# Kernel optimization log

Hardware: AMD Instinct MI355X
Metric: run time of the kernel (lower is better)

Reference implementation:

```python
import jax, jax.numpy as jnp
import numpy as np

N_GRID = 16       # n
CELL_SIDE = 2.0
LATENT = 16       # latent_dim (pooling_dim for type_='social')
HIDDEN = 128
OUT_DIM = 128
CONSTANT = 0.0
NUM_TRACKS = 1024


def setup_inputs() -> dict:
    key = jax.random.key(0)
    ks = jax.random.split(key, 6)
    T = NUM_TRACKS
    hidden_state = jax.random.normal(ks[0], (T, HIDDEN), jnp.float32)
    # positions spread over a ~20m scene; obs2 is obs1 plus a small step (velocity)
    obs1 = jax.random.uniform(ks[1], (T, 2), jnp.float32) * 20.0
    obs2 = obs1 + jax.random.normal(ks[2], (T, 2), jnp.float32) * 0.5
    W_enc = jax.random.normal(ks[3], (HIDDEN, LATENT), jnp.float32) / np.sqrt(HIDDEN)
    b_enc = jnp.zeros((LATENT,), jnp.float32)
    in_dim = N_GRID * N_GRID * LATENT  # 4096
    W_emb = jax.random.normal(ks[4], (in_dim, OUT_DIM), jnp.float32) / np.sqrt(in_dim)
    b_emb = jnp.zeros((OUT_DIM,), jnp.float32)
    return dict(hidden_state=hidden_state, obs1=obs1, obs2=obs2,
                W_enc=W_enc, b_enc=b_enc, W_emb=W_emb, b_emb=b_emb)


def _social_grid(hidden_state, obs2, W_enc, b_enc):
    T = obs2.shape[0]
    # NaN rows -> 0 (mask = isnan(obs).any(dim=1))
    obs = jnp.where(jnp.isnan(obs2).any(axis=1, keepdims=True), 0.0, obs2)
    # static off-diagonal neighbor indices: row i lists all j != i  [T, T-1]
    cols = np.broadcast_to(np.arange(T), (T, T))
    nbr = cols[~np.eye(T, dtype=bool)].reshape(T, T - 1)
    rel = obs[nbr] - obs[:, None, :]                 # [T, T-1, 2] obs[j]-obs[i]
    vals = hidden_state[nbr] @ W_enc + b_enc         # [T, T-1, LATENT]
    # grid cell coordinates (pool_size=1, front=False)
    oij = rel / CELL_SIDE + N_GRID / 2.0             # [T, T-1, 2]
    in_range = jnp.sum((oij < 0) | (oij >= N_GRID), axis=2) == 0  # [T, T-1]
    oij_i = jnp.where(in_range[..., None], oij, 0.0).astype(jnp.int32)
    vals = jnp.where(in_range[..., None], vals, CONSTANT)
    oi = oij_i[..., 0] * N_GRID + oij_i[..., 1]      # flat cell index [T, T-1]
    occ = jnp.full((T, N_GRID * N_GRID, LATENT), CONSTANT, vals.dtype)
    occ = occ.at[jnp.arange(T)[:, None], oi].set(vals)
    # [T, LATENT, n, n]; blur_size=1 and lp_pool with kernel=pool_size=1 are identity
    return jnp.transpose(occ, (0, 2, 1)).reshape(T, LATENT, N_GRID, N_GRID)


def reference(hidden_state, obs1, obs2, W_enc, b_enc, W_emb, b_emb):
    grid = _social_grid(hidden_state, obs2, W_enc, b_enc)
    T = grid.shape[0]
    flat = grid.reshape(T, -1)                       # [T, n*n*LATENT]
    return jax.nn.relu(flat @ W_emb + b_emb)         # [T, OUT_DIM]
```

## Files before the change

### kernel.cpp

```cpp
#include <hip/hip_runtime.h>
#include <hip/hip_bf16.h>
#include <math.h>

#define T_TRACKS 1024
#define HIDDEN 128
#define LATENT 16
#define NGRID 16
#define NCELLS 256
#define KDIM 4096
#define OUTD 128

typedef unsigned short ushort_t;
typedef __attribute__((ext_vector_type(8))) short frag_ab;
typedef __attribute__((ext_vector_type(4))) float f32x4;

static __device__ inline ushort_t f2bf(float x) {
    __hip_bfloat16 h = __float2bfloat16(x);
    return *reinterpret_cast<ushort_t*>(&h);
}

#define WS_VALS 0
#define WS_OWN  32768
#define WS_WT   557056
#define WS_PART 1605632
#define WS_NEED (1605632 + 8388608)

__global__ __launch_bounds__(256) void prep_kernel(const float* __restrict__ hidden,
                                                   const float* __restrict__ obs2,
                                                   const float* __restrict__ W_enc,
                                                   const float* __restrict__ b_enc,
                                                   const float* __restrict__ W_emb,
                                                   ushort_t* __restrict__ vals_t,
                                                   ushort_t* __restrict__ owner,
                                                   ushort_t* __restrict__ W_t) {
    const int b = blockIdx.x;
    const int tid = threadIdx.x;
    if (b < 64) {
        int idx = b * 256 + tid;
        int j = idx >> 4, l = idx & 15;
        const float* h = hidden + j * HIDDEN;
        float acc = b_enc[l];
#pragma unroll 8
        for (int k = 0; k < HIDDEN; k++) acc += h[k] * W_enc[k * LATENT + l];
        vals_t[l * T_TRACKS + j] = f2bf(acc);
    } else if (b < 320) {
        int idx = (b - 64) * 256 + tid;
        int kc = idx >> 7;
        int o = idx & 127;
        ushort_t tmp[8];
#pragma unroll
        for (int u = 0; u < 8; u++) tmp[u] = f2bf(W_emb[(kc * 8 + u) * OUTD + o]);
        *reinterpret_cast<uint4*>(W_t + o * KDIM + kc * 8) = *reinterpret_cast<uint4*>(tmp);
    } else {
        __shared__ float2 sobs[T_TRACKS];
        __shared__ int own[16][NCELLS];
        const int rbase = (b - 320) * 16;
        for (int q = tid; q < T_TRACKS; q += 256) {
            float2 o = reinterpret_cast<const float2*>(obs2)[q];
            if (isnan(o.x) || isnan(o.y)) { o.x = 0.0f; o.y = 0.0f; }
            sobs[q] = o;
        }
        for (int q = tid; q < 16 * NCELLS; q += 256) (&own[0][0])[q] = -1;
        __syncthreads();
        {
            const int r = tid & 15;
            const int i = rbase + r;
            const float oix = sobs[i].x, oiy = sobs[i].y;
            for (int j = tid >> 4; j < T_TRACKS; j += 16) {
                if (j == i) continue;
                float gx = (sobs[j].x - oix) * 0.5f + 8.0f;
                float gy = (sobs[j].y - oiy) * 0.5f + 8.0f;
                bool inr = (gx >= 0.0f) && (gx < 16.0f) && (gy >= 0.0f) && (gy < 16.0f);
                int c = inr ? ((int)gx * NGRID + (int)gy) : 0;
                atomicMax(&own[r][c], j);
            }
        }
        __syncthreads();
        for (int q = tid; q < 16 * NCELLS; q += 256) {
            int rr = q >> 8, c = q & 255;
            int j = own[rr][c];
            bool valid = (j >= 0);
            if (valid && c == 0) {
                float oix = sobs[rbase + rr].x, oiy = sobs[rbase + rr].y;
                float gx = (sobs[j].x - oix) * 0.5f + 8.0f;
                float gy = (sobs[j].y - oiy) * 0.5f + 8.0f;
                valid = (gx >= 0.0f) && (gx < 16.0f) && (gy >= 0.0f) && (gy < 16.0f);
            }
            owner[(rbase + rr) * NCELLS + c] = valid ? (ushort_t)(j + 1) : (ushort_t)0;
        }
    }
}

#define BK 128
#define LDSTR 136
__global__ __launch_bounds__(256) void gemm_kernel(const ushort_t* __restrict__ owner,
                                                   const ushort_t* __restrict__ vals_t,
                                                   const ushort_t* __restrict__ W_t,
                                                   float* __restrict__ partial) {
    const int tid = threadIdx.x;
    const int kt = blockIdx.x >> 4;
    const int mt = blockIdx.x & 15;
    const int wave = tid >> 6;
    const int lane = tid & 63;
    const int lrow = lane & 15;
    const int quad = lane >> 4;

    __shared__ ushort_t As[64 * LDSTR];
    __shared__ ushort_t Bs[128 * LDSTR];

    const ushort_t* vrow = vals_t + kt * T_TRACKS;

    f32x4 acc[8];
#pragma unroll
    for (int nt = 0; nt < 8; nt++) acc[nt] = (f32x4){0.f, 0.f, 0.f, 0.f};

    for (int chunk = 0; chunk < 2; chunk++) {
        const int c0 = chunk * BK;
        for (int q = tid; q < 2048; q += 256) {
            int r = q >> 5, c4 = (q & 31) * 4;
            ushort4 o4 = *reinterpret_cast<const ushort4*>(owner + (mt * 64 + r) * NCELLS + c0 + c4);
            ushort4 v;
            v.x = o4.x ? vrow[o4.x - 1] : (ushort_t)0;
            v.y = o4.y ? vrow[o4.y - 1] : (ushort_t)0;
            v.z = o4.z ? vrow[o4.z - 1] : (ushort_t)0;
            v.w = o4.w ? vrow[o4.w - 1] : (ushort_t)0;
            *reinterpret_cast<ushort4*>(As + r * LDSTR + c4) = v;
        }
        for (int g = tid; g < 2048; g += 256) {
            int n = g >> 4, cs = g & 15;
            uint4 v = *reinterpret_cast<const uint4*>(W_t + n * KDIM + kt * 256 + c0 + cs * 8);
            *reinterpret_cast<uint4*>(Bs + n * LDSTR + cs * 8) = v;
        }
        __syncthreads();
#pragma unroll
        for (int ks = 0; ks < 4; ks++) {
            const int koff = ks * 32 + quad * 8;
            frag_ab a = *reinterpret_cast<const frag_ab*>(&As[(wave * 16 + lrow) * LDSTR + koff]);
#pragma unroll
            for (int nt = 0; nt < 8; nt++) {
                frag_ab bfr = *reinterpret_cast<const frag_ab*>(&Bs[(nt * 16 + lrow) * LDSTR + koff]);
                acc[nt] = __builtin_amdgcn_mfma_f32_16x16x32_bf16(a, bfr, acc[nt], 0, 0, 0);
            }
        }
        __syncthreads();
    }
    float* pt = partial + (size_t)kt * (T_TRACKS * OUTD) + (mt * 64) * OUTD;
#pragma unroll
    for (int nt = 0; nt < 8; nt++) {
        int n = nt * 16 + lrow;
#pragma unroll
        for (int reg = 0; reg < 4; reg++) {
            int m = wave * 16 + quad * 4 + reg;
            pt[m * OUTD + n] = acc[nt][reg];
        }
    }
}

__global__ __launch_bounds__(256) void reduce_kernel(const float* __restrict__ partial,
                                                     const float* __restrict__ b_emb,
                                                     float* __restrict__ out) {
    int idx = blockIdx.x * 256 + threadIdx.x;
    const float4* p4 = reinterpret_cast<const float4*>(partial);
    float4 s = p4[idx];
#pragma unroll
    for (int kt = 1; kt < 16; kt++) {
        float4 v = p4[kt * 32768 + idx];
        s.x += v.x; s.y += v.y; s.z += v.z; s.w += v.w;
    }
    float4 bv = reinterpret_cast<const float4*>(b_emb)[idx & 31];
    float4 r;
    r.x = fmaxf(s.x + bv.x, 0.0f);
    r.y = fmaxf(s.y + bv.y, 0.0f);
    r.z = fmaxf(s.z + bv.z, 0.0f);
    r.w = fmaxf(s.w + bv.w, 0.0f);
    reinterpret_cast<float4*>(out)[idx] = r;
}

__global__ __launch_bounds__(256) void vals_kernel_f32(const float* __restrict__ hidden,
                                                       const float* __restrict__ W_enc,
                                                       const float* __restrict__ b_enc,
                                                       float* __restrict__ vals) {
    int idx = blockIdx.x * 256 + threadIdx.x;
    int j = idx >> 4, l = idx & 15;
    const float* h = hidden + j * HIDDEN;
    float acc = b_enc[l];
#pragma unroll 8
    for (int k = 0; k < HIDDEN; k++) acc += h[k] * W_enc[k * LATENT + l];
    vals[idx] = acc;
}

__global__ __launch_bounds__(256) void pool_kernel_f32(const float* __restrict__ obs2,
                                                       const float* __restrict__ vals,
                                                       const float* __restrict__ W_emb,
                                                       const float* __restrict__ b_emb,
                                                       float* __restrict__ out) {
    const int i = blockIdx.x;
    const int tid = threadIdx.x;
    __shared__ int owner[NCELLS];
    __shared__ float occ[NCELLS * LATENT];
    __shared__ float partial[OUTD];
    owner[tid] = -1;
    float oix = obs2[i * 2 + 0];
    float oiy = obs2[i * 2 + 1];
    if (isnan(oix) || isnan(oiy)) { oix = 0.0f; oiy = 0.0f; }
    __syncthreads();
    for (int j = tid; j < T_TRACKS; j += 256) {
        if (j == i) continue;
        float ox = obs2[j * 2 + 0], oy = obs2[j * 2 + 1];
        if (isnan(ox) || isnan(oy)) { ox = 0.0f; oy = 0.0f; }
        float gx = (ox - oix) * 0.5f + 8.0f;
        float gy = (oy - oiy) * 0.5f + 8.0f;
        bool inr = (gx >= 0.0f) && (gx < 16.0f) && (gy >= 0.0f) && (gy < 16.0f);
        int c = inr ? ((int)gx * NGRID + (int)gy) : 0;
        atomicMax(&owner[c], j);
    }
    __syncthreads();
    {
        int j = owner[tid];
        bool valid = false;
        if (j >= 0) {
            float ox = obs2[j * 2 + 0], oy = obs2[j * 2 + 1];
            if (isnan(ox) || isnan(oy)) { ox = 0.0f; oy = 0.0f; }
            float gx = (ox - oix) * 0.5f + 8.0f;
            float gy = (oy - oiy) * 0.5f + 8.0f;
            valid = (gx >= 0.0f) && (gx < 16.0f) && (gy >= 0.0f) && (gy < 16.0f);
        }
        const float* vj = vals + (j >= 0 ? j : 0) * LATENT;
#pragma unroll
        for (int l = 0; l < LATENT; l++) occ[tid * LATENT + l] = valid ? vj[l] : 0.0f;
    }
    __syncthreads();
    const int o = tid & (OUTD - 1);
    const int half = tid >> 7;
    const int cbase = half * 128;
    float acc = 0.0f;
    for (int c = cbase; c < cbase + 128; c++) {
#pragma unroll
        for (int l = 0; l < LATENT; l++)
            acc += occ[c * LATENT + l] * W_emb[(l * NCELLS + c) * OUTD + o];
    }
    if (half == 0) partial[o] = acc;
    __syncthreads();
    if (half == 1) out[i * OUTD + o] = fmaxf(acc + partial[o] + b_emb[o], 0.0f);
}

extern "C" void kernel_launch(void* const* d_in, const int* in_sizes, int n_in,
                              void* d_out, int out_size, void* d_ws, size_t ws_size,
                              hipStream_t stream) {
    const float* hidden = (const float*)d_in[0];
    const float* obs2   = (const float*)d_in[2];
    const float* W_enc  = (const float*)d_in[3];
    const float* b_enc  = (const float*)d_in[4];
    const float* W_emb  = (const float*)d_in[5];
    const float* b_emb  = (const float*)d_in[6];
    float* out = (float*)d_out;

    if (ws_size < (size_t)WS_NEED) {
        float* vals = (float*)d_ws;
        vals_kernel_f32<<<(T_TRACKS * LATENT) / 256, 256, 0, stream>>>(hidden, W_enc, b_enc, vals);
        pool_kernel_f32<<<T_TRACKS, 256, 0, stream>>>(obs2, vals, W_emb, b_emb, out);
        return;
    }

    char* ws = (char*)d_ws;
    ushort_t* vals_t = (ushort_t*)(ws + WS_VALS);
    ushort_t* owner  = (ushort_t*)(ws + WS_OWN);
    ushort_t* W_t    = (ushort_t*)(ws + WS_WT);
    float*    partial = (float*)(ws + WS_PART);

    prep_kernel<<<384, 256, 0, stream>>>(hidden, obs2, W_enc, b_enc, W_emb, vals_t, owner, W_t);
    gemm_kernel<<<256, 256, 0, stream>>>(owner, vals_t, W_t, partial);
    reduce_kernel<<<128, 256, 0, stream>>>(partial, b_emb, out);
}
```

Before: 96.53 us.

## Fuse prep, GEMM and reduce into one cooperative kernel with grid syncs

```diff
diff --git a/kernel.cpp b/kernel.cpp
--- a/kernel.cpp
+++ b/kernel.cpp
@@ -1,6 +1,9 @@
 #include <hip/hip_runtime.h>
+#include <hip/hip_cooperative_groups.h>
 #include <hip/hip_bf16.h>
 #include <math.h>
+
+namespace cg = cooperative_groups;
 
 #define T_TRACKS 1024
 #define HIDDEN 128
@@ -24,6 +27,163 @@
 #define WS_WT   557056
 #define WS_PART 1605632
 #define WS_NEED (1605632 + 8388608)
+
+__global__ __launch_bounds__(256, 4) void fused_kernel(const float* __restrict__ hidden,
+                                                       const float* __restrict__ obs2,
+                                                       const float* __restrict__ W_enc,
+                                                       const float* __restrict__ b_enc,
+                                                       const float* __restrict__ W_emb,
+                                                       const float* __restrict__ b_emb,
+                                                       ushort_t* __restrict__ vals_t,
+                                                       ushort_t* __restrict__ owner,
+                                                       ushort_t* __restrict__ W_t,
+                                                       float* __restrict__ partial,
+                                                       float* __restrict__ out) {
+    cg::grid_group grid = cg::this_grid();
+    const int b = blockIdx.x;
+    const int tid = threadIdx.x;
+
+    __shared__ __attribute__((aligned(16))) char smem_raw[39168];
+
+    if (b < 64) {
+        int idx = b * 256 + tid;
+        int j = idx >> 4, l = idx & 15;
+        const float* h = hidden + j * HIDDEN;
+        float acc = b_enc[l];
+#pragma unroll 8
+        for (int k = 0; k < HIDDEN; k++) acc += h[k] * W_enc[k * LATENT + l];
+        vals_t[l * T_TRACKS + j] = f2bf(acc);
+    } else if (b < 128) {
+        float2* sobs = reinterpret_cast<float2*>(smem_raw);
+        int* own = reinterpret_cast<int*>(smem_raw + 8192);
+        const int rbase = (b - 64) * 16;
+        for (int q = tid; q < T_TRACKS; q += 256) {
+            float2 o = reinterpret_cast<const float2*>(obs2)[q];
+            if (isnan(o.x) || isnan(o.y)) { o.x = 0.0f; o.y = 0.0f; }
+            sobs[q] = o;
+        }
+        for (int q = tid; q < 16 * NCELLS; q += 256) own[q] = -1;
+        __syncthreads();
+        {
+            const int r = tid & 15;
+            const int i = rbase + r;
+            const float oix = sobs[i].x, oiy = sobs[i].y;
+            for (int j = tid >> 4; j < T_TRACKS; j += 16) {
+                if (j == i) continue;
+                float gx = (sobs[j].x - oix) * 0.5f + 8.0f;
+                float gy = (sobs[j].y - oiy) * 0.5f + 8.0f;
+                bool inr = (gx >= 0.0f) && (gx < 16.0f) && (gy >= 0.0f) && (gy < 16.0f);
+                int c = inr ? ((int)gx * NGRID + (int)gy) : 0;
+                atomicMax(&own[r * NCELLS + c], j);
+            }
+        }
+        __syncthreads();
+        for (int q = tid; q < 16 * NCELLS; q += 256) {
+            int rr = q >> 8, c = q & 255;
+            int j = own[q];
+            bool valid = (j >= 0);
+            if (valid && c == 0) {
+                float oix = sobs[rbase + rr].x, oiy = sobs[rbase + rr].y;
+                float gx = (sobs[j].x - oix) * 0.5f + 8.0f;
+                float gy = (sobs[j].y - oiy) * 0.5f + 8.0f;
+                valid = (gx >= 0.0f) && (gx < 16.0f) && (gy >= 0.0f) && (gy < 16.0f);
+            }
+            owner[(rbase + rr) * NCELLS + c] = valid ? (ushort_t)(j + 1) : (ushort_t)0;
+        }
+    } else {
+        int idx = (b - 128) * 256 + tid;
+        if (idx < 65536) {
+            int kc = idx >> 7, o = idx & 127;
+            ushort_t tmp[8];
+#pragma unroll
+            for (int u = 0; u < 8; u++) tmp[u] = f2bf(W_emb[(kc * 8 + u) * OUTD + o]);
+            *reinterpret_cast<uint4*>(W_t + o * KDIM + kc * 8) = *reinterpret_cast<uint4*>(tmp);
+        }
+    }
+
+    grid.sync();
+
+    {
+        const int kt = b >> 6;
+        const int mt = b & 63;
+        const int wave = tid >> 6;
+        const int lane = tid & 63;
+        const int lrow = lane & 15;
+        const int quad = lane >> 4;
+
+        ushort_t* As = reinterpret_cast<ushort_t*>(smem_raw);
+        ushort_t* Bs = reinterpret_cast<ushort_t*>(smem_raw + 16 * 136 * 2);
+        const ushort_t* vrow = vals_t + kt * T_TRACKS;
+
+        f32x4 acc[2];
+        acc[0] = (f32x4){0.f, 0.f, 0.f, 0.f};
+        acc[1] = (f32x4){0.f, 0.f, 0.f, 0.f};
+
+        for (int chunk = 0; chunk < 2; chunk++) {
+            const int c0 = chunk * 128;
+            for (int q = tid; q < 512; q += 256) {
+                int r = q >> 5, c4 = (q & 31) * 4;
+                ushort4 o4 = *reinterpret_cast<const ushort4*>(owner + (mt * 16 + r) * NCELLS + c0 + c4);
+                ushort4 v;
+                v.x = o4.x ? vrow[o4.x - 1] : (ushort_t)0;
+                v.y = o4.y ? vrow[o4.y - 1] : (ushort_t)0;
+                v.z = o4.z ? vrow[o4.z - 1] : (ushort_t)0;
+                v.w = o4.w ? vrow[o4.w - 1] : (ushort_t)0;
+                *reinterpret_cast<ushort4*>(As + r * 136 + c4) = v;
+            }
+            for (int g = tid; g < 2048; g += 256) {
+                int n = g >> 4, cs = g & 15;
+                uint4 v = *reinterpret_cast<const uint4*>(W_t + n * KDIM + kt * 256 + c0 + cs * 8);
+                *reinterpret_cast<uint4*>(Bs + n * 136 + cs * 8) = v;
+            }
+            __syncthreads();
+#pragma unroll
+            for (int ks = 0; ks < 4; ks++) {
+                const int koff = ks * 32 + quad * 8;
+                frag_ab a = *reinterpret_cast<const frag_ab*>(&As[lrow * 136 + koff]);
+#pragma unroll
+                for (int nt2 = 0; nt2 < 2; nt2++) {
+                    int nrow = (wave * 2 + nt2) * 16 + lrow;
+                    frag_ab bfr = *reinterpret_cast<const frag_ab*>(&Bs[nrow * 136 + koff]);
+                    acc[nt2] = __builtin_amdgcn_mfma_f32_16x16x32_bf16(a, bfr, acc[nt2], 0, 0, 0);
+                }
+            }
+            __syncthreads();
+        }
+        float* pt = partial + (size_t)kt * (T_TRACKS * OUTD) + (mt * 16) * OUTD;
+#pragma unroll
+        for (int nt2 = 0; nt2 < 2; nt2++) {
+            int n = (wave * 2 + nt2) * 16 + lrow;
+#pragma unroll
+            for (int reg = 0; reg < 4; reg++) {
+                int m = quad * 4 + reg;
+                pt[m * OUTD + n] = acc[nt2][reg];
+            }
+        }
+    }
+
+    grid.sync();
+
+    {
+        int gid = b * 256 + tid;
+        if (gid < 32768) {
+            const float4* p4 = reinterpret_cast<const float4*>(partial);
+            float4 s = p4[gid];
+#pragma unroll
+            for (int kt = 1; kt < 16; kt++) {
+                float4 v = p4[kt * 32768 + gid];
+                s.x += v.x; s.y += v.y; s.z += v.z; s.w += v.w;
+            }
+            float4 bv = reinterpret_cast<const float4*>(b_emb)[gid & 31];
+            float4 r;
+            r.x = fmaxf(s.x + bv.x, 0.0f);
+            r.y = fmaxf(s.y + bv.y, 0.0f);
+            r.z = fmaxf(s.z + bv.z, 0.0f);
+            r.w = fmaxf(s.w + bv.w, 0.0f);
+            reinterpret_cast<float4*>(out)[gid] = r;
+        }
+    }
+}
 
 __global__ __launch_bounds__(256) void prep_kernel(const float* __restrict__ hidden,
                                                    const float* __restrict__ obs2,
@@ -91,7 +251,6 @@
     }
 }
 
-#define BK 128
 #define LDSTR 136
 __global__ __launch_bounds__(256) void gemm_kernel(const ushort_t* __restrict__ owner,
                                                    const ushort_t* __restrict__ vals_t,
@@ -115,7 +274,7 @@
     for (int nt = 0; nt < 8; nt++) acc[nt] = (f32x4){0.f, 0.f, 0.f, 0.f};
 
     for (int chunk = 0; chunk < 2; chunk++) {
-        const int c0 = chunk * BK;
+        const int c0 = chunk * 128;
         for (int q = tid; q < 2048; q += 256) {
             int r = q >> 5, c4 = (q & 31) * 4;
             ushort4 o4 = *reinterpret_cast<const ushort4*>(owner + (mt * 64 + r) * NCELLS + c0 + c4);
@@ -263,10 +422,17 @@
     }
 
     char* ws = (char*)d_ws;
-    ushort_t* vals_t = (ushort_t*)(ws + WS_VALS);
-    ushort_t* owner  = (ushort_t*)(ws + WS_OWN);
-    ushort_t* W_t    = (ushort_t*)(ws + WS_WT);
+    ushort_t* vals_t  = (ushort_t*)(ws + WS_VALS);
+    ushort_t* owner   = (ushort_t*)(ws + WS_OWN);
+    ushort_t* W_t     = (ushort_t*)(ws + WS_WT);
     float*    partial = (float*)(ws + WS_PART);
+
+    void* args[] = {(void*)&hidden, (void*)&obs2, (void*)&W_enc, (void*)&b_enc,
+                    (void*)&W_emb, (void*)&b_emb,
+                    (void*)&vals_t, (void*)&owner, (void*)&W_t, (void*)&partial, (void*)&out};
+    hipError_t err = hipLaunchCooperativeKernel((void*)fused_kernel, dim3(1024), dim3(256),
+                                                args, 0, stream);
+    if (err == hipSuccess) return;
 
     prep_kernel<<<384, 256, 0, stream>>>(hidden, obs2, W_enc, b_enc, W_emb, vals_t, owner, W_t);
     gemm_kernel<<<256, 256, 0, stream>>>(owner, vals_t, W_t, partial);
```

Measured after the change: 328.6 us. +240.5%, slower.

## Fuse split-K reduction into GEMM via last-block atomic counter, shrink M tile

Applied to the files above, without the earlier changes.

```diff
diff --git a/kernel.cpp b/kernel.cpp
--- a/kernel.cpp
+++ b/kernel.cpp
@@ -22,8 +22,9 @@
 #define WS_VALS 0
 #define WS_OWN  32768
 #define WS_WT   557056
-#define WS_PART 1605632
-#define WS_NEED (1605632 + 8388608)
+#define WS_CNT  1605632
+#define WS_PART 1605888
+#define WS_NEED (1605888 + 8388608)
 
 __global__ __launch_bounds__(256) void prep_kernel(const float* __restrict__ hidden,
                                                    const float* __restrict__ obs2,
@@ -32,10 +33,12 @@
                                                    const float* __restrict__ W_emb,
                                                    ushort_t* __restrict__ vals_t,
                                                    ushort_t* __restrict__ owner,
-                                                   ushort_t* __restrict__ W_t) {
+                                                   ushort_t* __restrict__ W_t,
+                                                   int* __restrict__ cnt) {
     const int b = blockIdx.x;
     const int tid = threadIdx.x;
     if (b < 64) {
+        if (b == 0 && tid < 64) cnt[tid] = 0;
         int idx = b * 256 + tid;
         int j = idx >> 4, l = idx & 15;
         const float* h = hidden + j * HIDDEN;
@@ -91,89 +94,104 @@
     }
 }
 
-#define BK 128
-#define LDSTR 136
-__global__ __launch_bounds__(256) void gemm_kernel(const ushort_t* __restrict__ owner,
-                                                   const ushort_t* __restrict__ vals_t,
-                                                   const ushort_t* __restrict__ W_t,
-                                                   float* __restrict__ partial) {
+__global__ __launch_bounds__(256, 4) void gemm_kernel(const ushort_t* __restrict__ owner,
+                                                      const ushort_t* __restrict__ vals_t,
+                                                      const ushort_t* __restrict__ W_t,
+                                                      const float* __restrict__ b_emb,
+                                                      float* __restrict__ partial,
+                                                      int* __restrict__ cnt,
+                                                      float* __restrict__ out) {
     const int tid = threadIdx.x;
-    const int kt = blockIdx.x >> 4;
-    const int mt = blockIdx.x & 15;
+    const int kt = blockIdx.x >> 6;
+    const int mt = blockIdx.x & 63;
     const int wave = tid >> 6;
     const int lane = tid & 63;
     const int lrow = lane & 15;
     const int quad = lane >> 4;
 
-    __shared__ ushort_t As[64 * LDSTR];
-    __shared__ ushort_t Bs[128 * LDSTR];
+    __shared__ ushort_t As[16 * 136];
+    __shared__ ushort_t Bs[128 * 136];
+    __shared__ int last;
 
     const ushort_t* vrow = vals_t + kt * T_TRACKS;
 
-    f32x4 acc[8];
-#pragma unroll
-    for (int nt = 0; nt < 8; nt++) acc[nt] = (f32x4){0.f, 0.f, 0.f, 0.f};
+    f32x4 acc[2];
+    acc[0] = (f32x4){0.f, 0.f, 0.f, 0.f};
+    acc[1] = (f32x4){0.f, 0.f, 0.f, 0.f};
 
     for (int chunk = 0; chunk < 2; chunk++) {
-        const int c0 = chunk * BK;
-        for (int q = tid; q < 2048; q += 256) {
+        const int c0 = chunk * 128;
+        for (int q = tid; q < 512; q += 256) {
             int r = q >> 5, c4 = (q & 31) * 4;
-            ushort4 o4 = *reinterpret_cast<const ushort4*>(owner + (mt * 64 + r) * NCELLS + c0 + c4);
+            ushort4 o4 = *reinterpret_cast<const ushort4*>(owner + (mt * 16 + r) * NCELLS + c0 + c4);
             ushort4 v;
             v.x = o4.x ? vrow[o4.x - 1] : (ushort_t)0;
             v.y = o4.y ? vrow[o4.y - 1] : (ushort_t)0;
             v.z = o4.z ? vrow[o4.z - 1] : (ushort_t)0;
             v.w = o4.w ? vrow[o4.w - 1] : (ushort_t)0;
-            *reinterpret_cast<ushort4*>(As + r * LDSTR + c4) = v;
+            *reinterpret_cast<ushort4*>(As + r * 136 + c4) = v;
         }
         for (int g = tid; g < 2048; g += 256) {
             int n = g >> 4, cs = g & 15;
             uint4 v = *reinterpret_cast<const uint4*>(W_t + n * KDIM + kt * 256 + c0 + cs * 8);
-            *reinterpret_cast<uint4*>(Bs + n * LDSTR + cs * 8) = v;
+            *reinterpret_cast<uint4*>(Bs + n * 136 + cs * 8) = v;
         }
         __syncthreads();
 #pragma unroll
         for (int ks = 0; ks < 4; ks++) {
             const int koff = ks * 32 + quad * 8;
-            frag_ab a = *reinterpret_cast<const frag_ab*>(&As[(wave * 16 + lrow) * LDSTR + koff]);
-#pragma unroll
-            for (int nt = 0; nt < 8; nt++) {
-                frag_ab bfr = *reinterpret_cast<const frag_ab*>(&Bs[(nt * 16 + lrow) * LDSTR + koff]);
-                acc[nt] = __builtin_amdgcn_mfma_f32_16x16x32_bf16(a, bfr, acc[nt], 0, 0, 0);
-            }
-        }
-        __syncthreads();
-    }
-    float* pt = partial + (size_t)kt * (T_TRACKS * OUTD) + (mt * 64) * OUTD;
-#pragma unroll
-    for (int nt = 0; nt < 8; nt++) {
-        int n = nt * 16 + lrow;
+            frag_ab a = *reinterpret_cast<const frag_ab*>(&As[lrow * 136 + koff]);
+#pragma unroll
+            for (int nt2 = 0; nt2 < 2; nt2++) {
+                int nrow = (wave * 2 + nt2) * 16 + lrow;
+                frag_ab bfr = *reinterpret_cast<const frag_ab*>(&Bs[nrow * 136 + koff]);
+                acc[nt2] = __builtin_amdgcn_mfma_f32_16x16x32_bf16(a, bfr, acc[nt2], 0, 0, 0);
+            }
+        }
+        __syncthreads();
+    }
+    float* pt = partial + (size_t)kt * (T_TRACKS * OUTD) + (mt * 16) * OUTD;
+#pragma unroll
+    for (int nt2 = 0; nt2 < 2; nt2++) {
+        int n = (wave * 2 + nt2) * 16 + lrow;
 #pragma unroll
         for (int reg = 0; reg < 4; reg++) {
-            int m = wave * 16 + quad * 4 + reg;
-            pt[m * OUTD + n] = acc[nt][reg];
-        }
-    }
-}
-
-__global__ __launch_bounds__(256) void reduce_kernel(const float* __restrict__ partial,
-                                                     const float* __restrict__ b_emb,
-                                                     float* __restrict__ out) {
-    int idx = blockIdx.x * 256 + threadIdx.x;
-    const float4* p4 = reinterpret_cast<const float4*>(partial);
-    float4 s = p4[idx];
-#pragma unroll
-    for (int kt = 1; kt < 16; kt++) {
-        float4 v = p4[kt * 32768 + idx];
-        s.x += v.x; s.y += v.y; s.z += v.z; s.w += v.w;
-    }
-    float4 bv = reinterpret_cast<const float4*>(b_emb)[idx & 31];
-    float4 r;
-    r.x = fmaxf(s.x + bv.x, 0.0f);
-    r.y = fmaxf(s.y + bv.y, 0.0f);
-    r.z = fmaxf(s.z + bv.z, 0.0f);
-    r.w = fmaxf(s.w + bv.w, 0.0f);
-    reinterpret_cast<float4*>(out)[idx] = r;
+            int m = quad * 4 + reg;
+            pt[m * OUTD + n] = acc[nt2][reg];
+        }
+    }
+
+    __threadfence();
+    __syncthreads();
+    if (tid == 0) {
+        int old = atomicAdd(&cnt[mt], 1);
+        last = (old == 15);
+    }
+    __syncthreads();
+    if (last) {
+        __threadfence();
+        const float4* p4 = reinterpret_cast<const float4*>(partial);
+        const float4* b4 = reinterpret_cast<const float4*>(b_emb);
+        float4* o4 = reinterpret_cast<float4*>(out);
+#pragma unroll
+        for (int u = 0; u < 2; u++) {
+            int e = tid + u * 256;
+            int base = mt * 512 + e;
+            float4 s = p4[base];
+#pragma unroll
+            for (int k2 = 1; k2 < 16; k2++) {
+                float4 v = p4[k2 * 32768 + base];
+                s.x += v.x; s.y += v.y; s.z += v.z; s.w += v.w;
+            }
+            float4 bv = b4[e & 31];
+            float4 r;
+            r.x = fmaxf(s.x + bv.x, 0.0f);
+            r.y = fmaxf(s.y + bv.y, 0.0f);
+            r.z = fmaxf(s.z + bv.z, 0.0f);
+            r.w = fmaxf(s.w + bv.w, 0.0f);
+            o4[base] = r;
+        }
+    }
 }
 
 __global__ __launch_bounds__(256) void vals_kernel_f32(const float* __restrict__ hidden,
@@ -263,12 +281,13 @@
     }
 
     char* ws = (char*)d_ws;
-    ushort_t* vals_t = (ushort_t*)(ws + WS_VALS);
-    ushort_t* owner  = (ushort_t*)(ws + WS_OWN);
-    ushort_t* W_t    = (ushort_t*)(ws + WS_WT);
+    ushort_t* vals_t  = (ushort_t*)(ws + WS_VALS);
+    ushort_t* owner   = (ushort_t*)(ws + WS_OWN);
+    ushort_t* W_t     = (ushort_t*)(ws + WS_WT);
+    int*      cnt     = (int*)(ws + WS_CNT);
     float*    partial = (float*)(ws + WS_PART);
 
-    prep_kernel<<<384, 256, 0, stream>>>(hidden, obs2, W_enc, b_enc, W_emb, vals_t, owner, W_t);
-    gemm_kernel<<<256, 256, 0, stream>>>(owner, vals_t, W_t, partial);
-    reduce_kernel<<<128, 256, 0, stream>>>(partial, b_emb, out);
-}
+    prep_kernel<<<384, 256, 0, stream>>>(hidden, obs2, W_enc, b_enc, W_emb,
+                                         vals_t, owner, W_t, cnt);
+    gemm_kernel<<<1024, 256, 0, stream>>>(owner, vals_t, W_t, b_emb, partial, cnt, out);
+}
```

Measured after the change: 193.6 us. +100.6%, slower.
